# Kernel optimization log

Hardware: AMD Instinct MI355X
Metric: run time of the kernel (lower is better)

The kernel has to match this reference:

```python
import jax, jax.numpy as jnp
import numpy as np
import math

B, S, D = 2, 1024, 2048
H, HD, ROT = 16, 128, 64
LQ, LKV = 1024, 512
ED, E, TOPK = 1024, 8, 2
EPS = 1e-6

def _rms(x, w):
    return w * (x * jax.lax.rsqrt(jnp.mean(x * x, axis=-1, keepdims=True) + EPS))

def _rope(x, cos, sin):
    # x: [B,S,H,R]; pairs are (even, odd) lanes, complex multiply expanded
    x0, x1 = x[..., 0::2], x[..., 1::2]
    c = cos[None, :, None, :]
    s = sin[None, :, None, :]
    out = jnp.stack([x0 * c - x1 * s, x0 * s + x1 * c], axis=-1)
    return out.reshape(x.shape)

def setup_inputs() -> dict:
    key = jax.random.key(0)
    ks = jax.random.split(key, 32)
    def rn(k, shape, fan):
        return jax.random.normal(k, shape, jnp.float32) / math.sqrt(fan)
    # RoPE tables
    theta = 10000.0 ** (-np.arange(0, ROT, 2, dtype=np.float32) / ROT)
    ang = np.arange(S, dtype=np.float32)[:, None] * theta[None, :]
    inp = {
        'x': jax.random.normal(ks[0], (B, S, D), jnp.float32),
        'freqs_cos': jnp.asarray(np.cos(ang)),
        'freqs_sin': jnp.asarray(np.sin(ang)),
        'w_norm1': jnp.ones((D,), jnp.float32),
        'w_lq': rn(ks[1], (D, LQ), D),
        'w_lkv': rn(ks[2], (D, LKV), D),
        'w_q': rn(ks[3], (LQ, H * HD), LQ),
        'w_k': rn(ks[4], (LKV, H * HD), LKV),
        'w_v': rn(ks[5], (LKV, H * HD), LKV),
        'w_qr': rn(ks[6], (LQ, H * ROT), LQ),
        'b_qr': jnp.zeros((H * ROT,), jnp.float32),
        'w_kr': rn(ks[7], (D, H * ROT), D),
        'b_kr': jnp.zeros((H * ROT,), jnp.float32),
        'w_o': rn(ks[8], (H * HD, D), H * HD),
        'b_o': jnp.zeros((D,), jnp.float32),
        'w_norm2': jnp.ones((D,), jnp.float32),
        'w_moe_norm': jnp.ones((D,), jnp.float32),
        'centroids': jax.random.normal(ks[9], (E, D), jnp.float32),
        'ws1': rn(ks[10], (D, ED), D),
        'bs1': jnp.zeros((ED,), jnp.float32),
        'ws2': rn(ks[11], (ED, D), ED),
        'bs2': jnp.zeros((D,), jnp.float32),
        'wr1': rn(ks[12], (E, D, ED), D),
        'br1': jnp.zeros((E, ED), jnp.float32),
        'wr2': rn(ks[13], (E, ED, D), ED),
        'br2': jnp.zeros((E, D), jnp.float32),
    }
    return inp

def reference(x, freqs_cos, freqs_sin, w_norm1, w_lq, w_lkv, w_q, w_k, w_v,
              w_qr, b_qr, w_kr, b_kr, w_o, b_o, w_norm2, w_moe_norm,
              centroids, ws1, bs1, ws2, bs2, wr1, br1, wr2, br2):
    # --- MLA attention with residual ---
    h = _rms(x, w_norm1)
    cq = h @ w_lq                      # [B,S,LQ]
    ckv = h @ w_lkv                    # [B,S,LKV]
    q = (cq @ w_q).reshape(B, S, H, HD)
    qr = _rope((cq @ w_qr + b_qr).reshape(B, S, H, ROT), freqs_cos, freqs_sin)
    k = (ckv @ w_k).reshape(B, S, H, HD)
    kr = _rope((h @ w_kr + b_kr).reshape(B, S, H, ROT), freqs_cos, freqs_sin)
    v = (ckv @ w_v).reshape(B, S, H, HD)
    qc = jnp.concatenate([q, qr], axis=-1)   # [B,S,H,HD+ROT]
    kc = jnp.concatenate([k, kr], axis=-1)
    scores = jnp.einsum('bqhd,bkhd->bhqk', qc, kc) / math.sqrt(HD + ROT)
    att = jax.nn.softmax(scores, axis=-1)
    o = jnp.einsum('bhqk,bkhd->bqhd', att, v).reshape(B, S, H * HD)
    x = x + (o @ w_o + b_o)
    # --- DeepSeekMoE (double RMSNorm per source) ---
    hn = _rms(_rms(x, w_norm2), w_moe_norm)
    shared = jax.nn.gelu((hn @ ws1 + bs1) @ ws2 + bs2, approximate=False)
    t = hn.reshape(-1, D)                      # [T,D], T=B*S
    aff = jax.nn.softmax(t @ centroids.T, axis=-1)  # [T,E]
    sc, idx = jax.lax.top_k(aff, TOPK)
    mask = jnp.zeros_like(aff).at[jnp.arange(t.shape[0])[:, None], idx].set(sc)
    mid = jnp.einsum('td,edf->tef', t, wr1) + br1          # [T,E,ED]
    out_e = jax.nn.gelu(jnp.einsum('tef,efd->ted', mid, wr2) + br2,
                        approximate=False)                  # [T,E,D]
    routed = jnp.einsum('te,ted->td', mask, out_e).reshape(B, S, D)
    return x + (hn + shared + routed)
```

## Files before the change

kernel.cpp:

```cpp
#include <hip/hip_runtime.h>
#include <math.h>

#define TT   2048
#define DM   2048
#define SEQ  1024
#define NH   16
#define NE   8
#define MB_  (1024*1024)
#define ATT_SCALE 0.07216878364870322f

typedef unsigned short u16;
typedef __attribute__((ext_vector_type(8))) short s8v;
typedef __attribute__((ext_vector_type(4))) float f4v;

__device__ __forceinline__ u16 f2bf(float f) {
  unsigned u = __builtin_bit_cast(unsigned, f);
  unsigned r = (u + 0x7fffu + ((u >> 16) & 1u)) >> 16;
  return (u16)r;
}
__device__ __forceinline__ float bf2f(u16 h) {
  return __builtin_bit_cast(float, (unsigned)h << 16);
}
__device__ __forceinline__ float gelu_f(float x) {
  return 0.5f * x * (1.0f + erff(x * 0.7071067811865476f));
}
__device__ __forceinline__ f4v mfma16(s8v a, s8v b, f4v c) {
  return __builtin_amdgcn_mfma_f32_16x16x32_bf16(a, b, c, 0, 0, 0);
}
__device__ __forceinline__ void gload16(const u16* g, u16* l) {
  __builtin_amdgcn_global_load_lds(
      (const __attribute__((address_space(1))) unsigned*)g,
      (__attribute__((address_space(3))) unsigned*)l, 16, 0, 0);
}

__global__ __launch_bounds__(256) void tcast_k(const float* __restrict__ src,
                                               u16* __restrict__ dst, int R, int C) {
  __shared__ float tile[32][33];
  const size_t bofs = (size_t)blockIdx.z * R * C;
  src += bofs; dst += bofs;
  const int r0 = blockIdx.y * 32, c0 = blockIdx.x * 32;
  const int t = threadIdx.x;
  const int tr = t >> 3, tc4 = (t & 7) * 4;
  float4 v = *(const float4*)&src[(size_t)(r0 + tr) * C + c0 + tc4];
  tile[tr][tc4 + 0] = v.x; tile[tr][tc4 + 1] = v.y;
  tile[tr][tc4 + 2] = v.z; tile[tr][tc4 + 3] = v.w;
  __syncthreads();
  ushort4 o;
  o.x = f2bf(tile[tc4 + 0][tr]);
  o.y = f2bf(tile[tc4 + 1][tr]);
  o.z = f2bf(tile[tc4 + 2][tr]);
  o.w = f2bf(tile[tc4 + 3][tr]);
  *(ushort4*)&dst[(size_t)(c0 + tr) * R + r0 + tc4] = o;
}

__global__ __launch_bounds__(256) void biasfill_k(float* __restrict__ bh,
                                                  float* __restrict__ bq,
                                                  const float* __restrict__ bkr,
                                                  const float* __restrict__ bqr) {
  const int i = blockIdx.x * 256 + threadIdx.x;
  if (i < 2560) bh[i] = (i >= 1536) ? bkr[i - 1536] : 0.f;
  bq[i] = (i >= 2048) ? bqr[i - 2048] : 0.f;
}

__device__ __forceinline__ float block_sum(float v, float* red) {
#pragma unroll
  for (int m = 32; m; m >>= 1) v += __shfl_xor(v, m);
  __syncthreads();
  if ((threadIdx.x & 63) == 0) red[threadIdx.x >> 6] = v;
  __syncthreads();
  return red[0] + red[1] + red[2] + red[3];
}

__global__ __launch_bounds__(256) void rmsb_k(const float* __restrict__ x,
                                              const float* __restrict__ w,
                                              u16* __restrict__ out) {
  __shared__ float red[4];
  const int t = blockIdx.x, tid = threadIdx.x;
  const float* xr = x + (size_t)t * DM;
  float4 v0 = *(const float4*)&xr[tid * 4];
  float4 v1 = *(const float4*)&xr[1024 + tid * 4];
  float ss = v0.x*v0.x + v0.y*v0.y + v0.z*v0.z + v0.w*v0.w
           + v1.x*v1.x + v1.y*v1.y + v1.z*v1.z + v1.w*v1.w;
  float s = block_sum(ss, red);
  float r = rsqrtf(s * (1.0f / DM) + 1e-6f);
  float4 w0 = *(const float4*)&w[tid * 4];
  float4 w1 = *(const float4*)&w[1024 + tid * 4];
  u16* orow = out + (size_t)t * DM;
  ushort4 o0, o1;
  o0.x = f2bf(v0.x*r*w0.x); o0.y = f2bf(v0.y*r*w0.y);
  o0.z = f2bf(v0.z*r*w0.z); o0.w = f2bf(v0.w*r*w0.w);
  o1.x = f2bf(v1.x*r*w1.x); o1.y = f2bf(v1.y*r*w1.y);
  o1.z = f2bf(v1.z*r*w1.z); o1.w = f2bf(v1.w*r*w1.w);
  *(ushort4*)&orow[tid * 4] = o0;
  *(ushort4*)&orow[1024 + tid * 4] = o1;
}

__global__ __launch_bounds__(256) void rms2_k(const float* __restrict__ x,
                                              const float* __restrict__ w2,
                                              const float* __restrict__ wm,
                                              float* __restrict__ outf,
                                              u16* __restrict__ outb) {
  __shared__ float red[4];
  const int t = blockIdx.x, tid = threadIdx.x;
  const float* xr = x + (size_t)t * DM;
  float4 v0 = *(const float4*)&xr[tid * 4];
  float4 v1 = *(const float4*)&xr[1024 + tid * 4];
  float ss = v0.x*v0.x + v0.y*v0.y + v0.z*v0.z + v0.w*v0.w
           + v1.x*v1.x + v1.y*v1.y + v1.z*v1.z + v1.w*v1.w;
  float s1 = block_sum(ss, red);
  float r1 = rsqrtf(s1 * (1.0f / DM) + 1e-6f);
  float4 a0 = *(const float4*)&w2[tid * 4];
  float4 a1 = *(const float4*)&w2[1024 + tid * 4];
  float4 y0 = make_float4(v0.x*r1*a0.x, v0.y*r1*a0.y, v0.z*r1*a0.z, v0.w*r1*a0.w);
  float4 y1 = make_float4(v1.x*r1*a1.x, v1.y*r1*a1.y, v1.z*r1*a1.z, v1.w*r1*a1.w);
  float ss2 = y0.x*y0.x + y0.y*y0.y + y0.z*y0.z + y0.w*y0.w
            + y1.x*y1.x + y1.y*y1.y + y1.z*y1.z + y1.w*y1.w;
  float s2 = block_sum(ss2, red);
  float r2 = rsqrtf(s2 * (1.0f / DM) + 1e-6f);
  float4 b0 = *(const float4*)&wm[tid * 4];
  float4 b1 = *(const float4*)&wm[1024 + tid * 4];
  float4 z0 = make_float4(y0.x*r2*b0.x, y0.y*r2*b0.y, y0.z*r2*b0.z, y0.w*r2*b0.w);
  float4 z1 = make_float4(y1.x*r2*b1.x, y1.y*r2*b1.y, y1.z*r2*b1.z, y1.w*r2*b1.w);
  float* orow = outf + (size_t)t * DM;
  *(float4*)&orow[tid * 4] = z0;
  *(float4*)&orow[1024 + tid * 4] = z1;
  u16* brow = outb + (size_t)t * DM;
  ushort4 o0, o1;
  o0.x = f2bf(z0.x); o0.y = f2bf(z0.y); o0.z = f2bf(z0.z); o0.w = f2bf(z0.w);
  o1.x = f2bf(z1.x); o1.y = f2bf(z1.y); o1.z = f2bf(z1.z); o1.w = f2bf(z1.w);
  *(ushort4*)&brow[tid * 4] = o0;
  *(ushort4*)&brow[1024 + tid * 4] = o1;
}

template <int ACT, bool BIAS, bool RES, int OUT>
__global__ __launch_bounds__(256) void bgemm_k(const u16* __restrict__ A, int lda,
                                               const u16* __restrict__ Bt, int ldb,
                                               void* __restrict__ C, int ldc, int K,
                                               const float* __restrict__ bias,
                                               const float* __restrict__ res, int ldr,
                                               void* __restrict__ C2, int ldc2, int nsplit) {
  __shared__ u16 As[128 * 64];
  __shared__ u16 Bs[128 * 64];
  const int tid = threadIdx.x;
  const int lane = tid & 63, w = tid >> 6;
  const int wr = w >> 1, wc = w & 1;
  const int l15 = lane & 15, l4 = lane >> 4;
  const int bm = blockIdx.y * 128, bn = blockIdx.x * 128;
  const int lrow = lane >> 3, lcol = (lane & 7) * 8;
  const u16* Abase = A + (size_t)(bm + w * 32 + lrow) * lda + lcol;
  const u16* Bbase = Bt + (size_t)(bn + w * 32 + lrow) * ldb + lcol;
  u16* AsW = As + (w * 32) * 64;
  u16* BsW = Bs + (w * 32) * 64;
  f4v acc[4][4] = {};
  for (int k0 = 0; k0 < K; k0 += 64) {
    __syncthreads();
#pragma unroll
    for (int j = 0; j < 4; ++j) {
      gload16(Abase + (size_t)j * 8 * lda + k0, AsW + j * 8 * 64);
      gload16(Bbase + (size_t)j * 8 * ldb + k0, BsW + j * 8 * 64);
    }
    __syncthreads();
#pragma unroll
    for (int kk = 0; kk < 2; ++kk) {
      s8v af[4], bfr[4];
#pragma unroll
      for (int m = 0; m < 4; ++m)
        af[m] = *(const s8v*)(As + (wr * 64 + m * 16 + l15) * 64 + kk * 32 + l4 * 8);
#pragma unroll
      for (int n = 0; n < 4; ++n)
        bfr[n] = *(const s8v*)(Bs + (wc * 64 + n * 16 + l15) * 64 + kk * 32 + l4 * 8);
#pragma unroll
      for (int m = 0; m < 4; ++m)
#pragma unroll
        for (int n = 0; n < 4; ++n)
          acc[m][n] = mfma16(af[m], bfr[n], acc[m][n]);
    }
  }
#pragma unroll
  for (int m = 0; m < 4; ++m) {
    const int row0 = bm + wr * 64 + m * 16 + l4 * 4;
#pragma unroll
    for (int n = 0; n < 4; ++n) {
      const int col = bn + wc * 64 + n * 16 + l15;
      f4v v = acc[m][n];
      float bv = BIAS ? bias[col] : 0.0f;
      if (OUT == 3 && col >= nsplit) {
        ushort4 o;
        o.x = f2bf(v[0] + bv); o.y = f2bf(v[1] + bv);
        o.z = f2bf(v[2] + bv); o.w = f2bf(v[3] + bv);
        *(ushort4*)((u16*)C2 + (size_t)(col - nsplit) * ldc2 + row0) = o;
      } else {
#pragma unroll
        for (int r = 0; r < 4; ++r) {
          float o = v[r] + bv;
          if (RES) o += res[(size_t)(row0 + r) * ldr + col];
          if (ACT == 1) o = gelu_f(o);
          if (OUT == 0) ((float*)C)[(size_t)(row0 + r) * ldc + col] = o;
          else          ((u16*)C)[(size_t)(row0 + r) * ldc + col] = f2bf(o);
        }
      }
    }
  }
}

template <bool GATHER, int ACT>
__global__ __launch_bounds__(256) void bgemm_grp_k(const u16* __restrict__ A, int lda,
                                                   const u16* __restrict__ BtAll, int K, int N,
                                                   u16* __restrict__ C,
                                                   const float* __restrict__ biasAll,
                                                   const int* __restrict__ counts,
                                                   const int* __restrict__ bases,
                                                   const int* __restrict__ entry_token) {
  const int e = blockIdx.z;
  const int cnt = counts[e];
  const int m0 = blockIdx.y * 128;
  if (m0 >= cnt) return;
  const int base = bases[e];
  const u16* Bt = BtAll + (size_t)e * K * N;
  const float* bias = biasAll + (size_t)e * N;
  __shared__ u16 As[128 * 64];
  __shared__ u16 Bs[128 * 64];
  const int tid = threadIdx.x;
  const int lane = tid & 63, w = tid >> 6;
  const int wr = w >> 1, wc = w & 1;
  const int l15 = lane & 15, l4 = lane >> 4;
  const int bn = blockIdx.x * 128;
  const int lrow = lane >> 3, lcol = (lane & 7) * 8;
  int aro[4];
#pragma unroll
  for (int j = 0; j < 4; ++j) {
    int rr = m0 + w * 32 + j * 8 + lrow;
    if (rr >= cnt) rr = cnt - 1;
    aro[j] = GATHER ? entry_token[base + rr] : (base + rr);
  }
  const u16* Bbase = Bt + (size_t)(bn + w * 32 + lrow) * K + lcol;
  u16* AsW = As + (w * 32) * 64;
  u16* BsW = Bs + (w * 32) * 64;
  f4v acc[4][4] = {};
  for (int k0 = 0; k0 < K; k0 += 64) {
    __syncthreads();
#pragma unroll
    for (int j = 0; j < 4; ++j) {
      gload16(A + (size_t)aro[j] * lda + k0 + lcol, AsW + j * 8 * 64);
      gload16(Bbase + (size_t)j * 8 * K + k0, BsW + j * 8 * 64);
    }
    __syncthreads();
#pragma unroll
    for (int kk = 0; kk < 2; ++kk) {
      s8v af[4], bfr[4];
#pragma unroll
      for (int m = 0; m < 4; ++m)
        af[m] = *(const s8v*)(As + (wr * 64 + m * 16 + l15) * 64 + kk * 32 + l4 * 8);
#pragma unroll
      for (int n = 0; n < 4; ++n)
        bfr[n] = *(const s8v*)(Bs + (wc * 64 + n * 16 + l15) * 64 + kk * 32 + l4 * 8);
#pragma unroll
      for (int m = 0; m < 4; ++m)
#pragma unroll
        for (int n = 0; n < 4; ++n)
          acc[m][n] = mfma16(af[m], bfr[n], acc[m][n]);
    }
  }
#pragma unroll
  for (int m = 0; m < 4; ++m) {
    const int rl0 = m0 + wr * 64 + m * 16 + l4 * 4;
#pragma unroll
    for (int n = 0; n < 4; ++n) {
      const int col = bn + wc * 64 + n * 16 + l15;
      f4v v = acc[m][n];
      float bv = bias[col];
#pragma unroll
      for (int r = 0; r < 4; ++r) {
        const int rl = rl0 + r;
        if (rl < cnt) {
          float o = v[r] + bv;
          if (ACT == 1) o = gelu_f(o);
          C[(size_t)(base + rl) * N + col] = f2bf(o);
        }
      }
    }
  }
}

__global__ __launch_bounds__(256) void ropeb_k(u16* __restrict__ buf, int ldb,
                                               const float* __restrict__ cosb,
                                               const float* __restrict__ sinb) {
  const int i = blockIdx.x * 256 + threadIdx.x;
  const int t = i >> 9;
  const int rem = i & 511;
  const int hh2 = rem >> 5, p = rem & 31;
  const int s = t & (SEQ - 1);
  const float c = cosb[s * 32 + p], sn = sinb[s * 32 + p];
  unsigned* ptr = (unsigned*)(buf + (size_t)t * ldb + hh2 * 64 + p * 2);
  unsigned vv = *ptr;
  float x0 = bf2f((u16)(vv & 0xffffu)), x1 = bf2f((u16)(vv >> 16));
  float y0 = x0 * c - x1 * sn, y1 = x0 * sn + x1 * c;
  *ptr = (unsigned)f2bf(y0) | ((unsigned)f2bf(y1) << 16);
}

__global__ __launch_bounds__(256) void attnb_k(const u16* __restrict__ qb, int ldq,
                                               const u16* __restrict__ qrb, int ldqr,
                                               const u16* __restrict__ kb, int ldk,
                                               const u16* __restrict__ krb, int ldkr,
                                               const u16* __restrict__ vt,
                                               u16* __restrict__ ob) {
  __shared__ u16 Ks[32 * 200];
  __shared__ u16 Vs[128 * 40];
  __shared__ u16 Ps[4][16 * 40];
  const int tid = threadIdx.x, lane = tid & 63, w = tid >> 6;
  const int l15 = lane & 15, l4 = lane >> 4;
  const int hh = blockIdx.y, bb = blockIdx.z;
  const int tbase = bb * SEQ;
  const int q0 = blockIdx.x * 64 + w * 16;
  const int qtok = tbase + q0 + l15;
  s8v aq[6];
#pragma unroll
  for (int kc = 0; kc < 4; ++kc)
    aq[kc] = *(const s8v*)(qb + (size_t)qtok * ldq + hh * 128 + kc * 32 + l4 * 8);
#pragma unroll
  for (int kc = 0; kc < 2; ++kc)
    aq[4 + kc] = *(const s8v*)(qrb + (size_t)qtok * ldqr + hh * 64 + kc * 32 + l4 * 8);
  f4v o[8] = {};
  float m_run[4] = {-1e30f, -1e30f, -1e30f, -1e30f};
  float l_run[4] = {0.f, 0.f, 0.f, 0.f};
  for (int kt = 0; kt < SEQ / 32; ++kt) {
    __syncthreads();
#pragma unroll
    for (int i = 0; i < 3; ++i) {
      int q = i * 256 + tid;
      int row = q / 24, c = q % 24;
      int tok = tbase + kt * 32 + row;
      s8v v;
      if (c < 16) v = *(const s8v*)(kb  + (size_t)tok * ldk + hh * 128 + c * 8);
      else        v = *(const s8v*)(krb + (size_t)tok * ldkr + hh * 64 + (c - 16) * 8);
      *(s8v*)(Ks + row * 200 + c * 8) = v;
    }
#pragma unroll
    for (int i = 0; i < 2; ++i) {
      int q = i * 256 + tid;
      int row = q >> 2, c = q & 3;
      s8v v = *(const s8v*)(vt + (size_t)(hh * 128 + row) * 2048 + tbase + kt * 32 + c * 8);
      *(s8v*)(Vs + row * 40 + c * 8) = v;
    }
    __syncthreads();
    f4v s0 = {}, s1 = {};
#pragma unroll
    for (int kc = 0; kc < 6; ++kc) {
      s8v bk0 = *(const s8v*)(Ks + l15 * 200 + kc * 32 + l4 * 8);
      s8v bk1 = *(const s8v*)(Ks + (16 + l15) * 200 + kc * 32 + l4 * 8);
      s0 = mfma16(aq[kc], bk0, s0);
      s1 = mfma16(aq[kc], bk1, s1);
    }
    float scf[4];
#pragma unroll
    for (int r = 0; r < 4; ++r) {
      float a = s0[r] * ATT_SCALE, b = s1[r] * ATT_SCALE;
      float mt = fmaxf(a, b);
#pragma unroll
      for (int msk = 1; msk < 16; msk <<= 1) mt = fmaxf(mt, __shfl_xor(mt, msk));
      float mn = fmaxf(m_run[r], mt);
      float p0 = __expf(a - mn), p1 = __expf(b - mn);
      float rs = p0 + p1;
#pragma unroll
      for (int msk = 1; msk < 16; msk <<= 1) rs += __shfl_xor(rs, msk);
      float sc = __expf(m_run[r] - mn);
      l_run[r] = l_run[r] * sc + rs;
      m_run[r] = mn;
      scf[r] = sc;
      int rq = l4 * 4 + r;
      Ps[w][rq * 40 + l15] = f2bf(p0);
      Ps[w][rq * 40 + 16 + l15] = f2bf(p1);
    }
#pragma unroll
    for (int dt = 0; dt < 8; ++dt) {
      o[dt][0] *= scf[0]; o[dt][1] *= scf[1];
      o[dt][2] *= scf[2]; o[dt][3] *= scf[3];
    }
    s8v pa = *(const s8v*)(&Ps[w][l15 * 40 + l4 * 8]);
#pragma unroll
    for (int dt = 0; dt < 8; ++dt) {
      s8v bv = *(const s8v*)(Vs + (dt * 16 + l15) * 40 + l4 * 8);
      o[dt] = mfma16(pa, bv, o[dt]);
    }
  }
  float linv[4];
#pragma unroll
  for (int r = 0; r < 4; ++r) linv[r] = 1.0f / l_run[r];
#pragma unroll
  for (int dt = 0; dt < 8; ++dt)
#pragma unroll
    for (int r = 0; r < 4; ++r)
      ob[(size_t)(tbase + q0 + l4 * 4 + r) * 2048 + hh * 128 + dt * 16 + l15] =
          f2bf(o[dt][r] * linv[r]);
}

__global__ __launch_bounds__(256) void router_k(const float* __restrict__ hn,
                                                const float* __restrict__ cent,
                                                int* __restrict__ topk_idx,
                                                float* __restrict__ topk_w,
                                                int* __restrict__ pos,
                                                int* __restrict__ counts) {
  const int t = blockIdx.x, tid = threadIdx.x;
  float p[NE] = {};
  const float* xr = hn + (size_t)t * DM;
  for (int d = tid * 4; d < DM; d += 1024) {
    float4 xv = *(const float4*)&xr[d];
#pragma unroll
    for (int e = 0; e < NE; ++e) {
      float4 cv = *(const float4*)&cent[e * DM + d];
      p[e] += xv.x * cv.x + xv.y * cv.y + xv.z * cv.z + xv.w * cv.w;
    }
  }
  __shared__ float wred[NE][4];
#pragma unroll
  for (int e = 0; e < NE; ++e) {
    float v = p[e];
#pragma unroll
    for (int m = 32; m; m >>= 1) v += __shfl_xor(v, m);
    if ((tid & 63) == 0) wred[e][tid >> 6] = v;
  }
  __syncthreads();
  if (tid == 0) {
    float lg[NE], mx = -3.0e38f;
    for (int e = 0; e < NE; ++e) {
      lg[e] = wred[e][0] + wred[e][1] + wred[e][2] + wred[e][3];
      mx = fmaxf(mx, lg[e]);
    }
    float pe[NE], sum = 0.f;
    for (int e = 0; e < NE; ++e) { pe[e] = expf(lg[e] - mx); sum += pe[e]; }
    const float inv = 1.f / sum;
    int i0 = 0; float v0 = -1.f;
    for (int e = 0; e < NE; ++e) { float a = pe[e] * inv; if (a > v0) { v0 = a; i0 = e; } }
    int i1 = 0; float v1 = -1.f;
    for (int e = 0; e < NE; ++e) { if (e == i0) continue; float a = pe[e] * inv; if (a > v1) { v1 = a; i1 = e; } }
    topk_idx[t * 2 + 0] = i0;
    topk_idx[t * 2 + 1] = i1;
    topk_w[t * 2 + 0] = v0;
    topk_w[t * 2 + 1] = v1;
    pos[t * 2 + 0] = atomicAdd(&counts[i0], 1);
    pos[t * 2 + 1] = atomicAdd(&counts[i1], 1);
  }
}

__global__ __launch_bounds__(256) void scatter_k(const int* __restrict__ topk_idx,
                                                 const int* __restrict__ pos,
                                                 const int* __restrict__ counts,
                                                 int* __restrict__ bases,
                                                 int* __restrict__ entry_token,
                                                 int* __restrict__ token_entry) {
  __shared__ int sb[NE];
  const int tid = threadIdx.x;
  if (tid == 0) {
    int acc = 0;
    for (int e = 0; e < NE; ++e) { sb[e] = acc; bases[e] = acc; acc += counts[e]; }
  }
  __syncthreads();
  for (int i = tid; i < TT * 2; i += 256) {
    const int e = topk_idx[i];
    const int entry = sb[e] + pos[i];
    entry_token[entry] = i >> 1;
    token_entry[i] = entry;
  }
}

__global__ __launch_bounds__(256) void combine_k(const float* __restrict__ x2,
                                                 const float* __restrict__ hn,
                                                 const float* __restrict__ sh,
                                                 const u16* __restrict__ oute,
                                                 const int* __restrict__ token_entry,
                                                 const float* __restrict__ topk_w,
                                                 float* __restrict__ out) {
  const int i = blockIdx.x * 256 + threadIdx.x;
  const int t = i >> 9;
  const int c = (i & 511) * 4;
  const int e0 = token_entry[t * 2 + 0], e1 = token_entry[t * 2 + 1];
  const float w0 = topk_w[t * 2 + 0], w1 = topk_w[t * 2 + 1];
  float4 a = *(const float4*)&x2[(size_t)t * DM + c];
  float4 b = *(const float4*)&hn[(size_t)t * DM + c];
  float4 s = *(const float4*)&sh[(size_t)t * DM + c];
  ushort4 u0 = *(const ushort4*)&oute[(size_t)e0 * DM + c];
  ushort4 u1 = *(const ushort4*)&oute[(size_t)e1 * DM + c];
  *(float4*)&out[(size_t)t * DM + c] =
      make_float4(a.x + b.x + s.x + w0 * bf2f(u0.x) + w1 * bf2f(u1.x),
                  a.y + b.y + s.y + w0 * bf2f(u0.y) + w1 * bf2f(u1.y),
                  a.z + b.z + s.z + w0 * bf2f(u0.z) + w1 * bf2f(u1.z),
                  a.w + b.w + s.w + w0 * bf2f(u0.w) + w1 * bf2f(u1.w));
}

extern "C" void kernel_launch(void* const* d_in, const int* in_sizes, int n_in,
                              void* d_out, int out_size, void* d_ws, size_t ws_size,
                              hipStream_t stream) {
  (void)in_sizes; (void)n_in; (void)out_size; (void)ws_size;
  const float* x       = (const float*)d_in[0];
  const float* fc      = (const float*)d_in[1];
  const float* fs      = (const float*)d_in[2];
  const float* w_norm1 = (const float*)d_in[3];
  const float* w_lq    = (const float*)d_in[4];
  const float* w_lkv   = (const float*)d_in[5];
  const float* w_q     = (const float*)d_in[6];
  const float* w_k     = (const float*)d_in[7];
  const float* w_v     = (const float*)d_in[8];
  const float* w_qr    = (const float*)d_in[9];
  const float* b_qr    = (const float*)d_in[10];
  const float* w_kr    = (const float*)d_in[11];
  const float* b_kr    = (const float*)d_in[12];
  const float* w_o     = (const float*)d_in[13];
  const float* b_o     = (const float*)d_in[14];
  const float* w_norm2 = (const float*)d_in[15];
  const float* w_moe   = (const float*)d_in[16];
  const float* cent    = (const float*)d_in[17];
  const float* ws1     = (const float*)d_in[18];
  const float* bs1     = (const float*)d_in[19];
  const float* ws2     = (const float*)d_in[20];
  const float* bs2     = (const float*)d_in[21];
  const float* wr1     = (const float*)d_in[22];
  const float* br1     = (const float*)d_in[23];
  const float* wr2     = (const float*)d_in[24];
  const float* br2     = (const float*)d_in[25];
  float* out = (float*)d_out;

  char* W = (char*)d_ws;
  u16* wt_h   = (u16*)(W + (size_t)0  * MB_);
  u16* wt_qqr = (u16*)(W + (size_t)10 * MB_);
  u16* wt_kv  = (u16*)(W + (size_t)16 * MB_);
  u16* wt_o   = (u16*)(W + (size_t)20 * MB_);
  u16* wt_s1  = (u16*)(W + (size_t)28 * MB_);
  u16* wt_s2  = (u16*)(W + (size_t)32 * MB_);
  u16* wt_r1  = (u16*)(W + (size_t)36 * MB_);
  u16* wt_r2  = (u16*)(W + (size_t)68 * MB_);
  u16* h_bf   = (u16*)(W + (size_t)100 * MB_);
  u16* hp     = (u16*)(W + (size_t)108 * MB_);
  u16* qp     = (u16*)(W + (size_t)118 * MB_);
  u16* kbuf   = (u16*)(W + (size_t)130 * MB_);
  u16* vbuf_t = (u16*)(W + (size_t)138 * MB_);
  u16* obuf   = (u16*)(W + (size_t)146 * MB_);
  float* x2   = (float*)(W + (size_t)100 * MB_);
  float* hn   = (float*)(W + (size_t)116 * MB_);
  u16* hn_bf  = (u16*)(W + (size_t)132 * MB_);
  u16* s1b    = (u16*)(W + (size_t)140 * MB_);
  float* shb  = (float*)(W + (size_t)144 * MB_);
  u16* midb   = (u16*)(W + (size_t)160 * MB_);
  u16* oute   = (u16*)(W + (size_t)168 * MB_);
  int* ip          = (int*)(W + (size_t)184 * MB_);
  int* counts      = ip;
  int* bases       = ip + 8;
  int* topk_idx    = ip + 16;
  int* pos         = ip + 16 + 4096;
  int* token_entry = ip + 16 + 8192;
  int* entry_token = ip + 16 + 12288;
  float* topk_w    = (float*)(ip + 16 + 16384);
  float* bias_h    = (float*)(ip + 16 + 20480);
  float* bias_q    = bias_h + 2560;

  tcast_k<<<dim3(32, 64), 256, 0, stream>>>(w_lq,  wt_h,                    2048, 1024);
  tcast_k<<<dim3(16, 64), 256, 0, stream>>>(w_lkv, wt_h + 1024 * 2048,      2048, 512);
  tcast_k<<<dim3(32, 64), 256, 0, stream>>>(w_kr,  wt_h + 1536 * 2048,      2048, 1024);
  tcast_k<<<dim3(64, 32), 256, 0, stream>>>(w_q,   wt_qqr,                  1024, 2048);
  tcast_k<<<dim3(32, 32), 256, 0, stream>>>(w_qr,  wt_qqr + 2048 * 1024,    1024, 1024);
  tcast_k<<<dim3(64, 16), 256, 0, stream>>>(w_k,   wt_kv,                   512,  2048);
  tcast_k<<<dim3(64, 16), 256, 0, stream>>>(w_v,   wt_kv + 2048 * 512,      512,  2048);
  tcast_k<<<dim3(64, 64), 256, 0, stream>>>(w_o,   wt_o,                    2048, 2048);
  tcast_k<<<dim3(32, 64), 256, 0, stream>>>(ws1,   wt_s1,                   2048, 1024);
  tcast_k<<<dim3(64, 32), 256, 0, stream>>>(ws2,   wt_s2,                   1024, 2048);
  tcast_k<<<dim3(32, 64, 8), 256, 0, stream>>>(wr1, wt_r1,                  2048, 1024);
  tcast_k<<<dim3(64, 32, 8), 256, 0, stream>>>(wr2, wt_r2,                  1024, 2048);
  biasfill_k<<<12, 256, 0, stream>>>(bias_h, bias_q, b_kr, b_qr);

  rmsb_k<<<TT, 256, 0, stream>>>(x, w_norm1, h_bf);
  bgemm_k<0, true, false, 1><<<dim3(20, 16), 256, 0, stream>>>(
      h_bf, 2048, wt_h, 2048, hp, 2560, 2048, bias_h, nullptr, 0, nullptr, 0, 0);
  bgemm_k<0, true, false, 1><<<dim3(24, 16), 256, 0, stream>>>(
      hp, 2560, wt_qqr, 1024, qp, 3072, 1024, bias_q, nullptr, 0, nullptr, 0, 0);
  bgemm_k<0, false, false, 3><<<dim3(32, 16), 256, 0, stream>>>(
      hp + 1024, 2560, wt_kv, 512, kbuf, 2048, 512, nullptr, nullptr, 0, vbuf_t, 2048, 2048);
  ropeb_k<<<4096, 256, 0, stream>>>(qp + 2048, 3072, fc, fs);
  ropeb_k<<<4096, 256, 0, stream>>>(hp + 1536, 2560, fc, fs);
  attnb_k<<<dim3(16, NH, 2), 256, 0, stream>>>(qp, 3072, qp + 2048, 3072,
                                               kbuf, 2048, hp + 1536, 2560, vbuf_t, obuf);
  bgemm_k<0, true, true, 0><<<dim3(16, 16), 256, 0, stream>>>(
      obuf, 2048, wt_o, 2048, x2, 2048, 2048, b_o, x, 2048, nullptr, 0, 0);
  rms2_k<<<TT, 256, 0, stream>>>(x2, w_norm2, w_moe, hn, hn_bf);
  bgemm_k<0, true, false, 1><<<dim3(8, 16), 256, 0, stream>>>(
      hn_bf, 2048, wt_s1, 2048, s1b, 1024, 2048, bs1, nullptr, 0, nullptr, 0, 0);
  bgemm_k<1, true, false, 0><<<dim3(16, 16), 256, 0, stream>>>(
      s1b, 1024, wt_s2, 1024, shb, 2048, 1024, bs2, nullptr, 0, nullptr, 0, 0);
  hipMemsetAsync(counts, 0, NE * sizeof(int), stream);
  router_k<<<TT, 256, 0, stream>>>(hn, cent, topk_idx, topk_w, pos, counts);
  scatter_k<<<1, 256, 0, stream>>>(topk_idx, pos, counts, bases, entry_token, token_entry);
  bgemm_grp_k<true, 0><<<dim3(8, 32, NE), 256, 0, stream>>>(
      hn_bf, 2048, wt_r1, 2048, 1024, midb, br1, counts, bases, entry_token);
  bgemm_grp_k<false, 1><<<dim3(16, 32, NE), 256, 0, stream>>>(
      midb, 1024, wt_r2, 1024, 2048, oute, br2, counts, bases, nullptr);
  combine_k<<<4096, 256, 0, stream>>>(x2, hn, shb, oute, token_entry, topk_w, out);
}
```

Before: 847.9 us.

## Double-buffer GEMM LDS tiles and batch weight-cast and RoPE launches

```diff
diff --git a/kernel.cpp b/kernel.cpp
--- a/kernel.cpp
+++ b/kernel.cpp
@@ -33,12 +33,26 @@
       (__attribute__((address_space(3))) unsigned*)l, 16, 0, 0);
 }
 
-__global__ __launch_bounds__(256) void tcast_k(const float* __restrict__ src,
-                                               u16* __restrict__ dst, int R, int C) {
+struct TD { const float* src; u16* dst; int R; int C; int startTile; };
+struct TDs { TD d[12]; };
+
+__global__ __launch_bounds__(256) void tcastb_k(TDs P) {
   __shared__ float tile[32][33];
-  const size_t bofs = (size_t)blockIdx.z * R * C;
-  src += bofs; dst += bofs;
-  const int r0 = blockIdx.y * 32, c0 = blockIdx.x * 32;
+  const int b = blockIdx.x;
+  int i = 0;
+#pragma unroll
+  for (int j = 1; j < 12; ++j) if (b >= P.d[j].startTile) i = j;
+  const float* src0 = P.d[i].src;
+  u16* dst0 = P.d[i].dst;
+  const int R = P.d[i].R, C = P.d[i].C;
+  const int local = b - P.d[i].startTile;
+  const int cpt = C >> 5;
+  const int ty = local / cpt, tx = local - ty * cpt;
+  const int r0g = ty * 32, c0 = tx * 32;
+  const int z = r0g / R;
+  const int r0 = r0g - z * R;
+  const float* src = src0 + (size_t)z * R * C;
+  u16* dst = dst0 + (size_t)z * R * C;
   const int t = threadIdx.x;
   const int tr = t >> 3, tc4 = (t & 7) * 4;
   float4 v = *(const float4*)&src[(size_t)(r0 + tr) * C + c0 + tc4];
@@ -133,14 +147,14 @@
 }
 
 template <int ACT, bool BIAS, bool RES, int OUT>
-__global__ __launch_bounds__(256) void bgemm_k(const u16* __restrict__ A, int lda,
-                                               const u16* __restrict__ Bt, int ldb,
-                                               void* __restrict__ C, int ldc, int K,
-                                               const float* __restrict__ bias,
-                                               const float* __restrict__ res, int ldr,
-                                               void* __restrict__ C2, int ldc2, int nsplit) {
-  __shared__ u16 As[128 * 64];
-  __shared__ u16 Bs[128 * 64];
+__global__ __launch_bounds__(256, 2) void bgemm_k(const u16* __restrict__ A, int lda,
+                                                  const u16* __restrict__ Bt, int ldb,
+                                                  void* __restrict__ C, int ldc, int K,
+                                                  const float* __restrict__ bias,
+                                                  const float* __restrict__ res, int ldr,
+                                                  void* __restrict__ C2, int ldc2, int nsplit) {
+  __shared__ u16 As[2][128 * 64];
+  __shared__ u16 Bs[2][128 * 64];
   const int tid = threadIdx.x;
   const int lane = tid & 63, w = tid >> 6;
   const int wr = w >> 1, wc = w & 1;
@@ -149,32 +163,42 @@
   const int lrow = lane >> 3, lcol = (lane & 7) * 8;
   const u16* Abase = A + (size_t)(bm + w * 32 + lrow) * lda + lcol;
   const u16* Bbase = Bt + (size_t)(bn + w * 32 + lrow) * ldb + lcol;
-  u16* AsW = As + (w * 32) * 64;
-  u16* BsW = Bs + (w * 32) * 64;
+  const int wofs = (w * 32) * 64;
   f4v acc[4][4] = {};
-  for (int k0 = 0; k0 < K; k0 += 64) {
-    __syncthreads();
-#pragma unroll
-    for (int j = 0; j < 4; ++j) {
-      gload16(Abase + (size_t)j * 8 * lda + k0, AsW + j * 8 * 64);
-      gload16(Bbase + (size_t)j * 8 * ldb + k0, BsW + j * 8 * 64);
-    }
-    __syncthreads();
+#pragma unroll
+  for (int j = 0; j < 4; ++j) {
+    gload16(Abase + (size_t)j * 8 * lda, &As[0][wofs + j * 8 * 64]);
+    gload16(Bbase + (size_t)j * 8 * ldb, &Bs[0][wofs + j * 8 * 64]);
+  }
+  __syncthreads();
+  const int nt = K >> 6;
+  int cur = 0;
+  for (int t = 0; t < nt; ++t) {
+    if (t + 1 < nt) {
+      const int k0 = (t + 1) << 6;
+#pragma unroll
+      for (int j = 0; j < 4; ++j) {
+        gload16(Abase + (size_t)j * 8 * lda + k0, &As[cur ^ 1][wofs + j * 8 * 64]);
+        gload16(Bbase + (size_t)j * 8 * ldb + k0, &Bs[cur ^ 1][wofs + j * 8 * 64]);
+      }
+    }
 #pragma unroll
     for (int kk = 0; kk < 2; ++kk) {
       s8v af[4], bfr[4];
 #pragma unroll
       for (int m = 0; m < 4; ++m)
-        af[m] = *(const s8v*)(As + (wr * 64 + m * 16 + l15) * 64 + kk * 32 + l4 * 8);
+        af[m] = *(const s8v*)(&As[cur][(wr * 64 + m * 16 + l15) * 64 + kk * 32 + l4 * 8]);
 #pragma unroll
       for (int n = 0; n < 4; ++n)
-        bfr[n] = *(const s8v*)(Bs + (wc * 64 + n * 16 + l15) * 64 + kk * 32 + l4 * 8);
+        bfr[n] = *(const s8v*)(&Bs[cur][(wc * 64 + n * 16 + l15) * 64 + kk * 32 + l4 * 8]);
 #pragma unroll
       for (int m = 0; m < 4; ++m)
 #pragma unroll
         for (int n = 0; n < 4; ++n)
           acc[m][n] = mfma16(af[m], bfr[n], acc[m][n]);
     }
+    __syncthreads();
+    cur ^= 1;
   }
 #pragma unroll
   for (int m = 0; m < 4; ++m) {
@@ -204,13 +228,13 @@
 }
 
 template <bool GATHER, int ACT>
-__global__ __launch_bounds__(256) void bgemm_grp_k(const u16* __restrict__ A, int lda,
-                                                   const u16* __restrict__ BtAll, int K, int N,
-                                                   u16* __restrict__ C,
-                                                   const float* __restrict__ biasAll,
-                                                   const int* __restrict__ counts,
-                                                   const int* __restrict__ bases,
-                                                   const int* __restrict__ entry_token) {
+__global__ __launch_bounds__(256, 2) void bgemm_grp_k(const u16* __restrict__ A, int lda,
+                                                      const u16* __restrict__ BtAll, int K, int N,
+                                                      u16* __restrict__ C,
+                                                      const float* __restrict__ biasAll,
+                                                      const int* __restrict__ counts,
+                                                      const int* __restrict__ bases,
+                                                      const int* __restrict__ entry_token) {
   const int e = blockIdx.z;
   const int cnt = counts[e];
   const int m0 = blockIdx.y * 128;
@@ -218,8 +242,8 @@
   const int base = bases[e];
   const u16* Bt = BtAll + (size_t)e * K * N;
   const float* bias = biasAll + (size_t)e * N;
-  __shared__ u16 As[128 * 64];
-  __shared__ u16 Bs[128 * 64];
+  __shared__ u16 As[2][128 * 64];
+  __shared__ u16 Bs[2][128 * 64];
   const int tid = threadIdx.x;
   const int lane = tid & 63, w = tid >> 6;
   const int wr = w >> 1, wc = w & 1;
@@ -234,32 +258,42 @@
     aro[j] = GATHER ? entry_token[base + rr] : (base + rr);
   }
   const u16* Bbase = Bt + (size_t)(bn + w * 32 + lrow) * K + lcol;
-  u16* AsW = As + (w * 32) * 64;
-  u16* BsW = Bs + (w * 32) * 64;
+  const int wofs = (w * 32) * 64;
   f4v acc[4][4] = {};
-  for (int k0 = 0; k0 < K; k0 += 64) {
-    __syncthreads();
-#pragma unroll
-    for (int j = 0; j < 4; ++j) {
-      gload16(A + (size_t)aro[j] * lda + k0 + lcol, AsW + j * 8 * 64);
-      gload16(Bbase + (size_t)j * 8 * K + k0, BsW + j * 8 * 64);
-    }
-    __syncthreads();
+#pragma unroll
+  for (int j = 0; j < 4; ++j) {
+    gload16(A + (size_t)aro[j] * lda + lcol, &As[0][wofs + j * 8 * 64]);
+    gload16(Bbase + (size_t)j * 8 * K, &Bs[0][wofs + j * 8 * 64]);
+  }
+  __syncthreads();
+  const int nt = K >> 6;
+  int cur = 0;
+  for (int t = 0; t < nt; ++t) {
+    if (t + 1 < nt) {
+      const int k0 = (t + 1) << 6;
+#pragma unroll
+      for (int j = 0; j < 4; ++j) {
+        gload16(A + (size_t)aro[j] * lda + k0 + lcol, &As[cur ^ 1][wofs + j * 8 * 64]);
+        gload16(Bbase + (size_t)j * 8 * K + k0, &Bs[cur ^ 1][wofs + j * 8 * 64]);
+      }
+    }
 #pragma unroll
     for (int kk = 0; kk < 2; ++kk) {
       s8v af[4], bfr[4];
 #pragma unroll
       for (int m = 0; m < 4; ++m)
-        af[m] = *(const s8v*)(As + (wr * 64 + m * 16 + l15) * 64 + kk * 32 + l4 * 8);
+        af[m] = *(const s8v*)(&As[cur][(wr * 64 + m * 16 + l15) * 64 + kk * 32 + l4 * 8]);
 #pragma unroll
       for (int n = 0; n < 4; ++n)
-        bfr[n] = *(const s8v*)(Bs + (wc * 64 + n * 16 + l15) * 64 + kk * 32 + l4 * 8);
+        bfr[n] = *(const s8v*)(&Bs[cur][(wc * 64 + n * 16 + l15) * 64 + kk * 32 + l4 * 8]);
 #pragma unroll
       for (int m = 0; m < 4; ++m)
 #pragma unroll
         for (int n = 0; n < 4; ++n)
           acc[m][n] = mfma16(af[m], bfr[n], acc[m][n]);
     }
+    __syncthreads();
+    cur ^= 1;
   }
 #pragma unroll
   for (int m = 0; m < 4; ++m) {
@@ -282,10 +316,15 @@
   }
 }
 
-__global__ __launch_bounds__(256) void ropeb_k(u16* __restrict__ buf, int ldb,
-                                               const float* __restrict__ cosb,
-                                               const float* __restrict__ sinb) {
-  const int i = blockIdx.x * 256 + threadIdx.x;
+__global__ __launch_bounds__(256) void ropeb2_k(u16* __restrict__ qbuf, int ldq,
+                                                u16* __restrict__ kbuf, int ldk,
+                                                const float* __restrict__ cosb,
+                                                const float* __restrict__ sinb) {
+  const int gi = blockIdx.x * 256 + threadIdx.x;
+  const int which = gi >> 20;
+  const int i = gi & ((1 << 20) - 1);
+  u16* buf = which ? kbuf : qbuf;
+  const int ldb = which ? ldk : ldq;
   const int t = i >> 9;
   const int rem = i & 511;
   const int hh2 = rem >> 5, p = rem & 31;
@@ -552,18 +591,20 @@
   float* bias_h    = (float*)(ip + 16 + 20480);
   float* bias_q    = bias_h + 2560;
 
-  tcast_k<<<dim3(32, 64), 256, 0, stream>>>(w_lq,  wt_h,                    2048, 1024);
-  tcast_k<<<dim3(16, 64), 256, 0, stream>>>(w_lkv, wt_h + 1024 * 2048,      2048, 512);
-  tcast_k<<<dim3(32, 64), 256, 0, stream>>>(w_kr,  wt_h + 1536 * 2048,      2048, 1024);
-  tcast_k<<<dim3(64, 32), 256, 0, stream>>>(w_q,   wt_qqr,                  1024, 2048);
-  tcast_k<<<dim3(32, 32), 256, 0, stream>>>(w_qr,  wt_qqr + 2048 * 1024,    1024, 1024);
-  tcast_k<<<dim3(64, 16), 256, 0, stream>>>(w_k,   wt_kv,                   512,  2048);
-  tcast_k<<<dim3(64, 16), 256, 0, stream>>>(w_v,   wt_kv + 2048 * 512,      512,  2048);
-  tcast_k<<<dim3(64, 64), 256, 0, stream>>>(w_o,   wt_o,                    2048, 2048);
-  tcast_k<<<dim3(32, 64), 256, 0, stream>>>(ws1,   wt_s1,                   2048, 1024);
-  tcast_k<<<dim3(64, 32), 256, 0, stream>>>(ws2,   wt_s2,                   1024, 2048);
-  tcast_k<<<dim3(32, 64, 8), 256, 0, stream>>>(wr1, wt_r1,                  2048, 1024);
-  tcast_k<<<dim3(64, 32, 8), 256, 0, stream>>>(wr2, wt_r2,                  1024, 2048);
+  TDs P;
+  P.d[0]  = {w_lq,  wt_h,               2048, 1024, 0};
+  P.d[1]  = {w_lkv, wt_h + 1024 * 2048, 2048, 512,  2048};
+  P.d[2]  = {w_kr,  wt_h + 1536 * 2048, 2048, 1024, 3072};
+  P.d[3]  = {w_q,   wt_qqr,             1024, 2048, 5120};
+  P.d[4]  = {w_qr,  wt_qqr + 2048*1024, 1024, 1024, 7168};
+  P.d[5]  = {w_k,   wt_kv,              512,  2048, 8192};
+  P.d[6]  = {w_v,   wt_kv + 2048*512,   512,  2048, 9216};
+  P.d[7]  = {w_o,   wt_o,               2048, 2048, 10240};
+  P.d[8]  = {ws1,   wt_s1,              2048, 1024, 14336};
+  P.d[9]  = {ws2,   wt_s2,              1024, 2048, 16384};
+  P.d[10] = {wr1,   wt_r1,              2048, 1024, 18432};
+  P.d[11] = {wr2,   wt_r2,              1024, 2048, 34816};
+  tcastb_k<<<51200, 256, 0, stream>>>(P);
   biasfill_k<<<12, 256, 0, stream>>>(bias_h, bias_q, b_kr, b_qr);
 
   rmsb_k<<<TT, 256, 0, stream>>>(x, w_norm1, h_bf);
@@ -573,8 +614,7 @@
       hp, 2560, wt_qqr, 1024, qp, 3072, 1024, bias_q, nullptr, 0, nullptr, 0, 0);
   bgemm_k<0, false, false, 3><<<dim3(32, 16), 256, 0, stream>>>(
       hp + 1024, 2560, wt_kv, 512, kbuf, 2048, 512, nullptr, nullptr, 0, vbuf_t, 2048, 2048);
-  ropeb_k<<<4096, 256, 0, stream>>>(qp + 2048, 3072, fc, fs);
-  ropeb_k<<<4096, 256, 0, stream>>>(hp + 1536, 2560, fc, fs);
+  ropeb2_k<<<8192, 256, 0, stream>>>(qp + 2048, 3072, hp + 1536, 2560, fc, fs);
   attnb_k<<<dim3(16, NH, 2), 256, 0, stream>>>(qp, 3072, qp + 2048, 3072,
                                                kbuf, 2048, hp + 1536, 2560, vbuf_t, obuf);
   bgemm_k<0, true, true, 0><<<dim3(16, 16), 256, 0, stream>>>(
```

Measured after the change: 820.9 us. 1.03x faster.
